# Kernel optimization log

Hardware: AMD Instinct MI355X
Metric: run time of the kernel (lower is better)

## Reference

```python
import jax, jax.numpy as jnp
import numpy as np

T, B, D, H, F, E = 2048, 2, 1024, 16, 4096, 8
HD = D // H


def layer_norm(x, g, b, eps=1e-5):
    m = x.mean(-1, keepdims=True)
    v = ((x - m) ** 2).mean(-1, keepdims=True)
    return (x - m) * jax.lax.rsqrt(v + eps) * g + b


def setup_inputs() -> dict:
    key = jax.random.key(0)
    ks = jax.random.split(key, 24)
    s = 0.02
    inp = {
        "x": jax.random.normal(ks[0], (T, B, D), jnp.float32),
        # self-attention (fairseq MultiheadAttention)
        "Wq": jax.random.normal(ks[1], (D, D), jnp.float32) * s,
        "bq": jnp.zeros((D,), jnp.float32),
        "Wk": jax.random.normal(ks[2], (D, D), jnp.float32) * s,
        "bk": jnp.zeros((D,), jnp.float32),
        "Wv": jax.random.normal(ks[3], (D, D), jnp.float32) * s,
        "bv": jnp.zeros((D,), jnp.float32),
        "Wo": jax.random.normal(ks[4], (D, D), jnp.float32) * s,
        "bo": jnp.zeros((D,), jnp.float32),
        "ln1_g": jnp.ones((D,), jnp.float32),
        "ln1_b": jnp.zeros((D,), jnp.float32),
        "ln2_g": jnp.ones((D,), jnp.float32),
        "ln2_b": jnp.zeros((D,), jnp.float32),
        # MoE: expert_centroids Linear(D -> E, bias=False) => weight [E, D]
        "cent": jax.random.normal(ks[5], (E, D), jnp.float32) * s,
        # per-expert MoESublayer params (base_sublayers=1)
        "e_ln_g": jnp.ones((E, D), jnp.float32),
        "e_ln_b": jnp.zeros((E, D), jnp.float32),
        "e_W1": jax.random.normal(ks[6], (E, D, F), jnp.float32) * s,
        "e_b1": jnp.zeros((E, F), jnp.float32),
        "e_W2": jax.random.normal(ks[7], (E, F, D), jnp.float32) * s,
        "e_b2": jnp.zeros((E, D), jnp.float32),
    }
    return inp


def reference(x, Wq, bq, Wk, bk, Wv, bv, Wo, bo, ln1_g, ln1_b, ln2_g, ln2_b,
              cent, e_ln_g, e_ln_b, e_W1, e_b1, e_W2, e_b2):
    # ---- self-attention block (pre-norm, causal) ----
    res = x  # [T,B,D]
    h = layer_norm(x, ln1_g, ln1_b)
    q = ((h @ Wq) + bq) * (HD ** -0.5)
    k = h @ Wk + bk
    v = h @ Wv + bv
    q = q.reshape(T, B, H, HD)
    k = k.reshape(T, B, H, HD)
    v = v.reshape(T, B, H, HD)
    scores = jnp.einsum('tbhd,sbhd->bhts', q, k)
    causal = jnp.tril(jnp.ones((T, T), bool))
    scores = jnp.where(causal, scores, -1e9)
    p = jax.nn.softmax(scores, axis=-1)
    a = jnp.einsum('bhts,sbhd->tbhd', p, v).reshape(T, B, D)
    x = res + (a @ Wo + bo)

    # ---- MoE block (pre-norm) ----
    res = x
    h = layer_norm(x, ln2_g, ln2_b)
    # MoELayer: transpose(0,1) then flatten -> [B*T, D] token-major by batch
    xs = h.transpose(1, 0, 2).reshape(B * T, D)
    logits = xs.astype(jnp.float32) @ cent.T  # fp32 gating, [N,E]
    assign = jnp.argmax(logits, axis=-1)      # greedy top-1 routing

    # single-device semantics: All2All identity; sort + inverse-sort cancel,
    # so out[t] = expert_{assign[t]}(xs[t]). Compute each expert densely and select.
    def sublayer(g, b, W1, b1, W2, b2):
        hh = jax.nn.relu(layer_norm(xs, g, b) @ W1 + b1)  # [N,F]
        return xs + hh @ W2 + b2                          # internal residual

    ys = jax.vmap(sublayer)(e_ln_g, e_ln_b, e_W1, e_b1, e_W2, e_b2)  # [E,N,D]
    moe_out = jnp.take_along_axis(ys, assign[None, :, None], axis=0)[0]  # [N,D]
    moe_out = moe_out.reshape(B, T, D).transpose(1, 0, 2)  # back to [T,B,D]

    return res + moe_out
```

## Files before the change

### kernel.cpp

```cpp
#include <hip/hip_runtime.h>
#include <hip/hip_bf16.h>
#include <math.h>

#define T_ 2048
#define B_ 2
#define D_ 1024
#define H_ 16
#define F_ 4096
#define E_ 8
#define N_ 4096
#define HD_ 64
#define PADROWS 5120

typedef __attribute__((ext_vector_type(8))) short short8_t;
typedef __attribute__((ext_vector_type(4))) float f32x4_t;
typedef __attribute__((ext_vector_type(16))) float f32x16_t;
typedef __attribute__((ext_vector_type(4))) unsigned u32x4_t;

__device__ __forceinline__ unsigned short f2bf(float f) {
    union { float f; unsigned u; } a; a.f = f;
    unsigned r = a.u + 0x7FFFu + ((a.u >> 16) & 1u);
    return (unsigned short)(r >> 16);
}

__device__ __forceinline__ unsigned cvtpk(float lo, float hi) {
    unsigned r;
    asm("v_cvt_pk_bf16_f32 %0, %1, %2" : "=v"(r) : "v"(lo), "v"(hi));
    return r;
}

__device__ __forceinline__ void glds16(const unsigned short* g, unsigned short* l) {
    __builtin_amdgcn_global_load_lds(
        (const __attribute__((address_space(1))) void*)g,
        (__attribute__((address_space(3))) void*)l, 16, 0, 0);
}

__device__ __forceinline__ void blockReduce2(float& a, float& b, float* sm) {
    #pragma unroll
    for (int m = 32; m; m >>= 1) { a += __shfl_xor(a, m); b += __shfl_xor(b, m); }
    const int w = threadIdx.x >> 6, l = threadIdx.x & 63;
    __syncthreads();
    if (l == 0) { sm[w] = a; sm[8 + w] = b; }
    __syncthreads();
    a = sm[0] + sm[1] + sm[2] + sm[3];
    b = sm[8] + sm[9] + sm[10] + sm[11];
}

__global__ __launch_bounds__(256) void k_transpose4(
    const float* __restrict__ Wq, const float* __restrict__ Wk,
    const float* __restrict__ Wv, const float* __restrict__ Wo,
    unsigned short* __restrict__ WqkvT, unsigned short* __restrict__ WoT) {
    __shared__ float tile[32][33];
    const int zi = blockIdx.z;
    const float* in = zi == 0 ? Wq : (zi == 1 ? Wk : (zi == 2 ? Wv : Wo));
    unsigned short* out = zi == 3 ? WoT : (WqkvT + (size_t)zi * 1024 * 1024);
    const int c0 = blockIdx.x * 32, r0 = blockIdx.y * 32;
    const int tx = threadIdx.x & 31, ty = threadIdx.x >> 5;
    #pragma unroll
    for (int i = 0; i < 32; i += 8)
        tile[ty + i][tx] = in[(size_t)(r0 + ty + i) * 1024 + c0 + tx];
    __syncthreads();
    const int c = threadIdx.x >> 3, rq = (threadIdx.x & 7) * 4;
    ushort4 v;
    v.x = f2bf(tile[rq + 0][c]);
    v.y = f2bf(tile[rq + 1][c]);
    v.z = f2bf(tile[rq + 2][c]);
    v.w = f2bf(tile[rq + 3][c]);
    *(ushort4*)(out + (size_t)(c0 + c) * 1024 + r0 + rq) = v;
}

__global__ __launch_bounds__(256) void k_transpose(const float* __restrict__ in,
                                                   unsigned short* __restrict__ out,
                                                   int R, int C) {
    __shared__ float tile[32][33];
    const int c0 = blockIdx.x * 32, r0 = blockIdx.y * 32;
    const size_t base = (size_t)blockIdx.z * R * C;
    in += base; out += base;
    const int tx = threadIdx.x & 31, ty = threadIdx.x >> 5;
    #pragma unroll
    for (int i = 0; i < 32; i += 8)
        tile[ty + i][tx] = in[(size_t)(r0 + ty + i) * C + c0 + tx];
    __syncthreads();
    const int c = threadIdx.x >> 3, rq = (threadIdx.x & 7) * 4;
    ushort4 v;
    v.x = f2bf(tile[rq + 0][c]);
    v.y = f2bf(tile[rq + 1][c]);
    v.z = f2bf(tile[rq + 2][c]);
    v.w = f2bf(tile[rq + 3][c]);
    *(ushort4*)(out + (size_t)(c0 + c) * R + r0 + rq) = v;
}

__global__ __launch_bounds__(256) void k_transpose_v(const unsigned short* __restrict__ in,
                                                     unsigned short* __restrict__ out) {
    const int bh = blockIdx.x;
    const int t0 = blockIdx.y * 128;
    const int tid = threadIdx.x;
    const int hd = tid & 63;
    const size_t ib = (size_t)bh * T_ * HD_;
    const size_t ob = (size_t)bh * HD_ * T_;
    for (int tb = tid >> 6; tb < 16; tb += 4) {
        const int t = t0 + tb * 8;
        short8_t v;
        #pragma unroll
        for (int k = 0; k < 8; ++k)
            v[k] = (short)in[ib + (size_t)(t + k) * HD_ + hd];
        *(short8_t*)(out + ob + (size_t)hd * T_ + t) = v;
    }
}

__global__ __launch_bounds__(256) void k_ln_x2(const float* __restrict__ x,
                                               const float* __restrict__ g,
                                               const float* __restrict__ b,
                                               const float* __restrict__ bo,
                                               unsigned short* __restrict__ out,
                                               float* __restrict__ x2,
                                               int* __restrict__ counts, int* __restrict__ cursor,
                                               int* __restrict__ perm) {
    __shared__ float sm[16];
    const int row = blockIdx.x, tid = threadIdx.x;
    if (row == 0) {
        if (tid < E_) { counts[tid] = 0; cursor[tid] = 0; }
        for (int i = tid; i < PADROWS; i += 256) perm[i] = -1;
    }
    const float4 v = *(const float4*)(x + (size_t)row * D_ + tid * 4);
    float s1 = v.x + v.y + v.z + v.w;
    float s2 = v.x * v.x + v.y * v.y + v.z * v.z + v.w * v.w;
    blockReduce2(s1, s2, sm);
    const float mean = s1 * (1.f / D_);
    const float inv  = rsqrtf(s2 * (1.f / D_) - mean * mean + 1e-5f);
    const float4 gg = *(const float4*)(g + tid * 4);
    const float4 bb = *(const float4*)(b + tid * 4);
    unsigned long long pk =
          (unsigned long long)f2bf((v.x - mean) * inv * gg.x + bb.x)
        | ((unsigned long long)f2bf((v.y - mean) * inv * gg.y + bb.y) << 16)
        | ((unsigned long long)f2bf((v.z - mean) * inv * gg.z + bb.z) << 32)
        | ((unsigned long long)f2bf((v.w - mean) * inv * gg.w + bb.w) << 48);
    *(unsigned long long*)(out + (size_t)row * D_ + tid * 4) = pk;
    const float4 bv = *(const float4*)(bo + tid * 4);
    float4 o; o.x = v.x + bv.x; o.y = v.y + bv.y; o.z = v.z + bv.z; o.w = v.w + bv.w;
    *(float4*)(x2 + (size_t)row * D_ + tid * 4) = o;
}

__global__ __launch_bounds__(256) void k_init_out(const float* __restrict__ x2u,
                                                  const float* __restrict__ eb2,
                                                  const int* __restrict__ assign,
                                                  float* __restrict__ out) {
    const int row = blockIdx.x, tid = threadIdx.x;
    const int e = assign[row];
    const size_t idx = (size_t)row * D_ + tid * 4;
    const float4 v = *(const float4*)(x2u + idx);
    const float4 b = *(const float4*)(eb2 + (size_t)e * D_ + tid * 4);
    float4 o; o.x = v.x + b.x; o.y = v.y + b.y; o.z = v.z + b.z; o.w = v.w + b.w;
    *(float4*)(out + idx) = o;
}

__device__ __forceinline__ void gemm_core(const unsigned short* ap0, const unsigned short* ap1,
                                          const unsigned short* bp0, const unsigned short* bp1,
                                          int K, unsigned short* Als, unsigned short* Bls,
                                          f32x4_t (&acc)[4][4]) {
    const int tid = threadIdx.x, w = tid >> 6, l = tid & 63;
    const int wm = (w >> 1) * 64, wn = (w & 1) * 64;
    const int fr = l & 15, fg = (l >> 4) * 8;
    const int fgs = fg ^ (((fr >> 1) & 3) << 3);
    f32x4_t z4 = {0.f, 0.f, 0.f, 0.f};
    #pragma unroll
    for (int m = 0; m < 4; m++)
        #pragma unroll
        for (int n = 0; n < 4; n++) acc[m][n] = z4;
    glds16(ap0, Als + w * 512);
    glds16(ap1, Als + (w + 4) * 512);
    glds16(bp0, Bls + w * 512);
    glds16(bp1, Bls + (w + 4) * 512);
    ap0 += 32; ap1 += 32; bp0 += 32; bp1 += 32;
    glds16(ap0, Als + 4096 + w * 512);
    glds16(ap1, Als + 4096 + (w + 4) * 512);
    glds16(bp0, Bls + 4096 + w * 512);
    glds16(bp1, Bls + 4096 + (w + 4) * 512);
    ap0 += 32; ap1 += 32; bp0 += 32; bp1 += 32;
    unsigned c0 = 0, c1 = 4096, c2 = 8192;
    const int nk = K >> 5;
    for (int kt = 0; kt < nk; ++kt) {
        if (kt < nk - 1) asm volatile("s_waitcnt vmcnt(4)" ::: "memory");
        else             asm volatile("s_waitcnt vmcnt(0)" ::: "memory");
        __builtin_amdgcn_s_barrier();
        __builtin_amdgcn_sched_barrier(0);
        if (kt + 2 < nk) {
            glds16(ap0, Als + c2 + w * 512);
            glds16(ap1, Als + c2 + (w + 4) * 512);
            glds16(bp0, Bls + c2 + w * 512);
            glds16(bp1, Bls + c2 + (w + 4) * 512);
            ap0 += 32; ap1 += 32; bp0 += 32; bp1 += 32;
        }
        short8_t a[4], b[4];
        #pragma unroll
        for (int m = 0; m < 4; m++) a[m] = *(const short8_t*)(Als + c0 + (wm + m * 16 + fr) * 32 + fgs);
        #pragma unroll
        for (int n = 0; n < 4; n++) b[n] = *(const short8_t*)(Bls + c0 + (wn + n * 16 + fr) * 32 + fgs);
        __builtin_amdgcn_s_setprio(1);
        #pragma unroll
        for (int m = 0; m < 4; m++)
            #pragma unroll
            for (int n = 0; n < 4; n++)
                acc[m][n] = __builtin_amdgcn_mfma_f32_16x16x32_bf16(a[m], b[n], acc[m][n], 0, 0, 0);
        __builtin_amdgcn_s_setprio(0);
        const unsigned t = c0; c0 = c1; c1 = c2; c2 = t;
    }
}

__global__ __launch_bounds__(256) void k_gemm_qkv(
    const unsigned short* __restrict__ A, const unsigned short* __restrict__ BT,
    const float* __restrict__ bq, const float* __restrict__ bk, const float* __restrict__ bv,
    unsigned short* __restrict__ Qb, unsigned short* __restrict__ Kb, unsigned short* __restrict__ Vb) {
    __shared__ unsigned short Als[12288], Bls[12288];
    const int tid = threadIdx.x, w = tid >> 6, l = tid & 63;
    const int col0 = blockIdx.x * 128, row0 = blockIdx.y * 128;
    const int r0s = w * 16 + (l >> 2), r1s = 64 + w * 16 + (l >> 2);
    const int cs = ((l & 3) ^ ((l >> 3) & 3)) * 8;
    const unsigned short* ap0 = A + (size_t)(row0 + r0s) * D_ + cs;
    const unsigned short* ap1 = A + (size_t)(row0 + r1s) * D_ + cs;
    const unsigned short* bp0 = BT + (size_t)(col0 + r0s) * D_ + cs;
    const unsigned short* bp1 = BT + (size_t)(col0 + r1s) * D_ + cs;
    f32x4_t acc[4][4];
    gemm_core(ap0, ap1, bp0, bp1, D_, Als, Bls, acc);
    const int wm = (w >> 1) * 64, wn = (w & 1) * 64, fr = l & 15, fg4 = l >> 4;
    #pragma unroll
    for (int n = 0; n < 4; n++) {
        const int gcol = col0 + wn + n * 16 + fr;
        const int which = gcol >> 10, dc = gcol & 1023;
        const float bias = which == 0 ? bq[dc] : (which == 1 ? bk[dc] : bv[dc]);
        unsigned short* dst = which == 0 ? Qb : (which == 1 ? Kb : Vb);
        const int hh = dc >> 6, hd = dc & 63;
        #pragma unroll
        for (int m = 0; m < 4; m++)
            #pragma unroll
            for (int rr = 0; rr < 4; rr++) {
                const int grow = row0 + wm + m * 16 + fg4 * 4 + rr;
                float v = acc[m][n][rr] + bias;
                if (which == 0) v *= 0.1803368801111204f;
                const int t = grow >> 1, bb = grow & 1;
                dst[((size_t)(bb * H_ + hh) * T_ + t) * HD_ + hd] = f2bf(v);
            }
    }
}

__global__ __launch_bounds__(256) void k_attn(const unsigned short* __restrict__ Qb,
                                              const unsigned short* __restrict__ Kb,
                                              const unsigned short* __restrict__ Vt,
                                              unsigned short* __restrict__ aout) {
    __shared__ unsigned short Kl[3 * 4096];
    __shared__ unsigned short Vl[3 * 4096];
    const int id = blockIdx.x;
    const int qt = (id < 256) ? (15 - (id & 15)) : (id & 15);
    const int bh = (id >> 4) & 31;
    const int tid = threadIdx.x, w = tid >> 6, l = tid & 63;
    const int q5 = l & 31, hi = l >> 5, l7 = l & 7;
    const int row0 = w * 8 + (l >> 3);
    const int swz = ((l & 7) ^ (l >> 3)) * 8;
    const size_t base = (size_t)bh * T_ * HD_;
    const unsigned short* Qp = Qb + base;
    const unsigned short* kps = Kb + base + (size_t)row0 * HD_ + swz;
    const unsigned short* vps = Vt + base + (size_t)row0 * T_ + swz;
    const int qw0 = qt * 128 + w * 32;
    const int q = qw0 + q5;

    short8_t aq[4];
    #pragma unroll
    for (int khd = 0; khd < 4; ++khd)
        aq[khd] = *(const short8_t*)(Qp + (size_t)q * HD_ + khd * 16 + hi * 8);

    f32x16_t accO0, accO1;
    #pragma unroll
    for (int i = 0; i < 16; ++i) { accO0[i] = 0.f; accO1[i] = 0.f; }
    float mrun = -1e30f, lrun = 0.f;

    const int niter = (qt + 1) * 2;

#define STAGE_KV(t, b) { \
    const size_t ko = (size_t)(t) * 64 * HD_; const int vo = (t) * 64; \
    glds16(kps + ko,            Kl + (b) + w * 512); \
    glds16(kps + ko + 32 * HD_, Kl + (b) + 2048 + w * 512); \
    glds16(vps + vo,            Vl + (b) + w * 512); \
    glds16(vps + vo + 32 * T_,  Vl + (b) + 2048 + w * 512); }

    STAGE_KV(0, 0);
    STAGE_KV(1, 4096);
    unsigned c0 = 0, c1 = 4096, c2 = 8192;

    for (int it = 0; it < niter; ++it) {
        if (it < niter - 1) asm volatile("s_waitcnt vmcnt(4)" ::: "memory");
        else                asm volatile("s_waitcnt vmcnt(0)" ::: "memory");
        __builtin_amdgcn_s_barrier();
        __builtin_amdgcn_sched_barrier(0);
        if (it + 2 < niter) STAGE_KV(it + 2, c2);
        const int s0 = it * 64;
        if (s0 <= qw0 + 31) {
            const unsigned short* KT = Kl + c0;
            const unsigned short* VT = Vl + c0;

            f32x16_t st0, st1;
            #pragma unroll
            for (int i = 0; i < 16; ++i) { st0[i] = 0.f; st1[i] = 0.f; }
            __builtin_amdgcn_s_setprio(1);
            #pragma unroll
            for (int khd = 0; khd < 4; ++khd) {
                const int cb = (khd * 16 + hi * 8) ^ (l7 * 8);
                const short8_t k0 = *(const short8_t*)(KT + q5 * 64 + cb);
                const short8_t k1 = *(const short8_t*)(KT + (32 + q5) * 64 + cb);
                st0 = __builtin_amdgcn_mfma_f32_32x32x16_bf16(k0, aq[khd], st0, 0, 0, 0);
                st1 = __builtin_amdgcn_mfma_f32_32x32x16_bf16(k1, aq[khd], st1, 0, 0, 0);
            }
            __builtin_amdgcn_s_setprio(0);

            const bool domask = (s0 + 63 > qw0);
            float pmax = -3e38f;
            if (domask) {
                #pragma unroll
                for (int r = 0; r < 16; ++r) {
                    const int kv0 = s0 + (r & 3) + 8 * (r >> 2) + 4 * hi;
                    float v0 = st0[r], v1 = st1[r];
                    if (kv0 > q)      v0 = -1e30f;
                    if (kv0 + 32 > q) v1 = -1e30f;
                    st0[r] = v0; st1[r] = v1;
                    pmax = fmaxf(fmaxf(pmax, v0), v1);
                }
            } else {
                #pragma unroll
                for (int r = 0; r < 16; ++r)
                    pmax = fmaxf(fmaxf(pmax, st0[r]), st1[r]);
            }
            pmax = fmaxf(pmax, __shfl_xor(pmax, 32));

            if (!__all(pmax - mrun <= 8.0f)) {
                const float mnew = fmaxf(mrun, pmax);
                const float scl = exp2f(mrun - mnew);
                lrun *= scl;
                #pragma unroll
                for (int i = 0; i < 16; ++i) { accO0[i] *= scl; accO1[i] *= scl; }
                mrun = mnew;
            }

            float pt0[16], pt1[16];
            float rs0 = 0.f, rs1 = 0.f;
            #pragma unroll
            for (int r = 0; r < 16; ++r) {
                pt0[r] = exp2f(st0[r] - mrun);
                pt1[r] = exp2f(st1[r] - mrun);
                rs0 += pt0[r]; rs1 += pt1[r];
            }
            float rs = rs0 + rs1;
            rs += __shfl_xor(rs, 32);
            lrun += rs;

            unsigned Wp[2][4][2];
            #pragma unroll
            for (int b = 0; b < 4; ++b) {
                Wp[0][b][0] = cvtpk(pt0[4 * b + 0], pt0[4 * b + 1]);
                Wp[0][b][1] = cvtpk(pt0[4 * b + 2], pt0[4 * b + 3]);
                Wp[1][b][0] = cvtpk(pt1[4 * b + 0], pt1[4 * b + 1]);
                Wp[1][b][1] = cvtpk(pt1[4 * b + 2], pt1[4 * b + 3]);
            }

            __builtin_amdgcn_s_setprio(1);
            #pragma unroll
            for (int ks = 0; ks < 4; ++ks) {
                const int t = ks >> 1, b0 = (ks & 1) * 2;
                const unsigned ownA0 = Wp[t][b0][0],     ownA1 = Wp[t][b0][1];
                const unsigned ownB0 = Wp[t][b0 + 1][0], ownB1 = Wp[t][b0 + 1][1];
                const unsigned send0 = hi ? ownA0 : ownB0;
                const unsigned send1 = hi ? ownA1 : ownB1;
                const unsigned recv0 = __shfl_xor(send0, 32);
                const unsigned recv1 = __shfl_xor(send1, 32);
                u32x4_t wds;
                wds[0] = hi ? recv0 : ownA0;
                wds[1] = hi ? recv1 : ownA1;
                wds[2] = hi ? ownB0 : recv0;
                wds[3] = hi ? ownB1 : recv1;
                const short8_t pfrag = __builtin_bit_cast(short8_t, wds);
                const int cb = (ks * 16 + hi * 8) ^ (l7 * 8);
                const short8_t v0 = *(const short8_t*)(VT + q5 * 64 + cb);
                const short8_t v1 = *(const short8_t*)(VT + (32 + q5) * 64 + cb);
                accO0 = __builtin_amdgcn_mfma_f32_32x32x16_bf16(v0, pfrag, accO0, 0, 0, 0);
                accO1 = __builtin_amdgcn_mfma_f32_32x32x16_bf16(v1, pfrag, accO1, 0, 0, 0);
            }
            __builtin_amdgcn_s_setprio(0);
        }
        const unsigned tb = c0; c0 = c1; c1 = c2; c2 = tb;
    }
#undef STAGE_KV

    const float linv = 1.f / lrun;
    const int bidx = bh >> 4, hidx = bh & 15;
    unsigned short* orow = aout + (size_t)(q * B_ + bidx) * D_ + hidx * 64;
    #pragma unroll
    for (int g = 0; g < 4; ++g) {
        const int hd0 = 8 * g + 4 * hi;
        unsigned long long pk0 =
              (unsigned long long)f2bf(accO0[4 * g + 0] * linv)
            | ((unsigned long long)f2bf(accO0[4 * g + 1] * linv) << 16)
            | ((unsigned long long)f2bf(accO0[4 * g + 2] * linv) << 32)
            | ((unsigned long long)f2bf(accO0[4 * g + 3] * linv) << 48);
        *(unsigned long long*)(orow + hd0) = pk0;
        unsigned long long pk1 =
              (unsigned long long)f2bf(accO1[4 * g + 0] * linv)
            | ((unsigned long long)f2bf(accO1[4 * g + 1] * linv) << 16)
            | ((unsigned long long)f2bf(accO1[4 * g + 2] * linv) << 32)
            | ((unsigned long long)f2bf(accO1[4 * g + 3] * linv) << 48);
        *(unsigned long long*)(orow + 32 + hd0) = pk1;
    }
}

__global__ __launch_bounds__(256) void k_gemm_o(
    const unsigned short* __restrict__ A, const unsigned short* __restrict__ BT,
    float* __restrict__ x2) {
    __shared__ unsigned short Als[12288], Bls[12288];
    const int tid = threadIdx.x, w = tid >> 6, l = tid & 63;
    const int row0 = blockIdx.x * 128, col0 = blockIdx.y * 128;
    const int kc = blockIdx.z * 512;
    const int r0s = w * 16 + (l >> 2), r1s = 64 + w * 16 + (l >> 2);
    const int cs = ((l & 3) ^ ((l >> 3) & 3)) * 8;
    const unsigned short* ap0 = A + (size_t)(row0 + r0s) * D_ + kc + cs;
    const unsigned short* ap1 = A + (size_t)(row0 + r1s) * D_ + kc + cs;
    const unsigned short* bp0 = BT + (size_t)(col0 + r0s) * D_ + kc + cs;
    const unsigned short* bp1 = BT + (size_t)(col0 + r1s) * D_ + kc + cs;
    f32x4_t acc[4][4];
    gemm_core(ap0, ap1, bp0, bp1, 512, Als, Bls, acc);
    const int wm = (w >> 1) * 64, wn = (w & 1) * 64, fr = l & 15, fg4 = l >> 4;
    #pragma unroll
    for (int n = 0; n < 4; n++) {
        const int gcol = col0 + wn + n * 16 + fr;
        #pragma unroll
        for (int m = 0; m < 4; m++)
            #pragma unroll
            for (int rr = 0; rr < 4; rr++) {
                const int grow = row0 + wm + m * 16 + fg4 * 4 + rr;
                atomicAdd(&x2[(size_t)grow * D_ + gcol], acc[m][n][rr]);
            }
    }
}

__global__ __launch_bounds__(256) void k_ln2_gate(
    float* __restrict__ x2, const float* __restrict__ g2, const float* __restrict__ b2,
    const float* __restrict__ cent, const float* __restrict__ eg, const float* __restrict__ eb,
    unsigned short* __restrict__ z, int* __restrict__ assign, int* __restrict__ counts) {
    __shared__ float sm[48];
    const int row = blockIdx.x, tid = threadIdx.x;
    const int w = tid >> 6, l = tid & 63;
    float* xr = x2 + (size_t)row * D_;
    const float4 v = *(const float4*)(xr + tid * 4);
    float s1 = v.x + v.y + v.z + v.w;
    float s2 = v.x * v.x + v.y * v.y + v.z * v.z + v.w * v.w;
    blockReduce2(s1, s2, sm);
    const float mean = s1 * (1.f / D_);
    const float inv  = rsqrtf(s2 * (1.f / D_) - mean * mean + 1e-5f);
    const float4 gg = *(const float4*)(g2 + tid * 4), bb = *(const float4*)(b2 + tid * 4);
    float4 u;
    u.x = (v.x - mean) * inv * gg.x + bb.x;
    u.y = (v.y - mean) * inv * gg.y + bb.y;
    u.z = (v.z - mean) * inv * gg.z + bb.z;
    u.w = (v.w - mean) * inv * gg.w + bb.w;
    float p[E_];
    #pragma unroll
    for (int e = 0; e < E_; e++) {
        const float4 c = *(const float4*)(cent + (size_t)e * D_ + tid * 4);
        p[e] = u.x * c.x + u.y * c.y + u.z * c.z + u.w * c.w;
    }
    #pragma unroll
    for (int m = 32; m; m >>= 1)
        #pragma unroll
        for (int e = 0; e < E_; e++) p[e] += __shfl_xor(p[e], m);
    __syncthreads();
    if (l == 0) {
        #pragma unroll
        for (int e = 0; e < E_; e++) sm[16 + e * 4 + w] = p[e];
    }
    __syncthreads();
    int best = 0; float bl = -1e30f;
    #pragma unroll
    for (int e = 0; e < E_; e++) {
        const float le = sm[16 + e * 4] + sm[16 + e * 4 + 1] + sm[16 + e * 4 + 2] + sm[16 + e * 4 + 3];
        if (le > bl) { bl = le; best = e; }
    }
    float t1 = u.x + u.y + u.z + u.w;
    float t2 = u.x * u.x + u.y * u.y + u.z * u.z + u.w * u.w;
    blockReduce2(t1, t2, sm);
    const float m2   = t1 * (1.f / D_);
    const float inv2 = rsqrtf(t2 * (1.f / D_) - m2 * m2 + 1e-5f);
    const float4 egv = *(const float4*)(eg + (size_t)best * D_ + tid * 4);
    const float4 ebv = *(const float4*)(eb + (size_t)best * D_ + tid * 4);
    unsigned long long pk =
          (unsigned long long)f2bf((u.x - m2) * inv2 * egv.x + ebv.x)
        | ((unsigned long long)f2bf((u.y - m2) * inv2 * egv.y + ebv.y) << 16)
        | ((unsigned long long)f2bf((u.z - m2) * inv2 * egv.z + ebv.z) << 32)
        | ((unsigned long long)f2bf((u.w - m2) * inv2 * egv.w + ebv.w) << 48);
    *(unsigned long long*)(z + (size_t)row * D_ + tid * 4) = pk;
    float4 xu; xu.x = v.x + u.x; xu.y = v.y + u.y; xu.z = v.z + u.z; xu.w = v.w + u.w;
    *(float4*)(xr + tid * 4) = xu;
    if (tid == 0) { assign[row] = best; atomicAdd(&counts[best], 1); }
}

__global__ void k_offsets(const int* counts, int* pad_off) {
    if (threadIdx.x == 0) {
        int o = 0; pad_off[0] = 0;
        for (int e = 0; e < E_; e++) { o += ((counts[e] + 127) >> 7) << 7; pad_off[e + 1] = o; }
    }
}

__global__ void k_scatter(const int* assign, const int* pad_off, int* cursor, int* perm) {
    const int r = blockIdx.x * 256 + threadIdx.x;
    if (r >= N_) return;
    const int e = assign[r];
    const int pos = pad_off[e] + atomicAdd(&cursor[e], 1);
    perm[pos] = r;
}

__global__ __launch_bounds__(256) void k_gemm_e1(
    const unsigned short* __restrict__ z, const unsigned short* __restrict__ W1T,
    const float* __restrict__ eb1, const int* __restrict__ pad_off,
    const int* __restrict__ perm, unsigned short* __restrict__ Y1) {
    __shared__ unsigned short Als[12288], Bls[12288];
    const int tid = threadIdx.x, w = tid >> 6, l = tid & 63;
    const int col0 = blockIdx.x * 128, row0 = blockIdx.y * 128;
    if (row0 >= pad_off[E_]) return;
    int e = 0;
    while (row0 >= pad_off[e + 1]) e++;
    const int r0s = w * 16 + (l >> 2), r1s = 64 + w * 16 + (l >> 2);
    const int cs = ((l & 3) ^ ((l >> 3) & 3)) * 8;
    int pr0 = perm[row0 + r0s]; if (pr0 < 0) pr0 = 0;
    int pr1 = perm[row0 + r1s]; if (pr1 < 0) pr1 = 0;
    const unsigned short* ap0 = z + (size_t)pr0 * D_ + cs;
    const unsigned short* ap1 = z + (size_t)pr1 * D_ + cs;
    const unsigned short* BTe = W1T + (size_t)e * F_ * D_;
    const unsigned short* bp0 = BTe + (size_t)(col0 + r0s) * D_ + cs;
    const unsigned short* bp1 = BTe + (size_t)(col0 + r1s) * D_ + cs;
    f32x4_t acc[4][4];
    gemm_core(ap0, ap1, bp0, bp1, D_, Als, Bls, acc);
    const float* b1e = eb1 + (size_t)e * F_;
    const int wm = (w >> 1) * 64, wn = (w & 1) * 64, fr = l & 15, fg4 = l >> 4;
    #pragma unroll
    for (int n = 0; n < 4; n++) {
        const int gcol = col0 + wn + n * 16 + fr;
        const float bias = b1e[gcol];
        #pragma unroll
        for (int m = 0; m < 4; m++)
            #pragma unroll
            for (int rr = 0; rr < 4; rr++) {
                const int grow = row0 + wm + m * 16 + fg4 * 4 + rr;
                Y1[(size_t)grow * F_ + gcol] = f2bf(fmaxf(acc[m][n][rr] + bias, 0.f));
            }
    }
}

__global__ __launch_bounds__(256) void k_gemm_e2(
    const unsigned short* __restrict__ Y1, const unsigned short* __restrict__ W2T,
    const int* __restrict__ pad_off, const int* __restrict__ perm,
    float* __restrict__ out) {
    __shared__ unsigned short Als[12288], Bls[12288];
    const int tid = threadIdx.x, w = tid >> 6, l = tid & 63;
    const int row0 = blockIdx.x * 128, col0 = blockIdx.y * 128;
    const int kc = blockIdx.z * 2048;
    if (row0 >= pad_off[E_]) return;
    int e = 0;
    while (row0 >= pad_off[e + 1]) e++;
    const int r0s = w * 16 + (l >> 2), r1s = 64 + w * 16 + (l >> 2);
    const int cs = ((l & 3) ^ ((l >> 3) & 3)) * 8;
    const unsigned short* ap0 = Y1 + (size_t)(row0 + r0s) * F_ + kc + cs;
    const unsigned short* ap1 = Y1 + (size_t)(row0 + r1s) * F_ + kc + cs;
    const unsigned short* BTe = W2T + (size_t)e * D_ * F_;
    const unsigned short* bp0 = BTe + (size_t)(col0 + r0s) * F_ + kc + cs;
    const unsigned short* bp1 = BTe + (size_t)(col0 + r1s) * F_ + kc + cs;
    f32x4_t acc[4][4];
    gemm_core(ap0, ap1, bp0, bp1, 2048, Als, Bls, acc);
    const int wm = (w >> 1) * 64, wn = (w & 1) * 64, fr = l & 15, fg4 = l >> 4;
    #pragma unroll
    for (int n = 0; n < 4; n++) {
        const int gcol = col0 + wn + n * 16 + fr;
        #pragma unroll
        for (int m = 0; m < 4; m++)
            #pragma unroll
            for (int rr = 0; rr < 4; rr++) {
                const int grow = row0 + wm + m * 16 + fg4 * 4 + rr;
                const int rdst = perm[grow];
                if (rdst >= 0)
                    atomicAdd(&out[(size_t)rdst * D_ + gcol], acc[m][n][rr]);
            }
    }
}

extern "C" void kernel_launch(void* const* d_in, const int* in_sizes, int n_in,
                              void* d_out, int out_size, void* d_ws, size_t ws_size,
                              hipStream_t stream) {
    const float* x    = (const float*)d_in[0];
    const float* Wq   = (const float*)d_in[1];
    const float* bq   = (const float*)d_in[2];
    const float* Wk   = (const float*)d_in[3];
    const float* bk   = (const float*)d_in[4];
    const float* Wv   = (const float*)d_in[5];
    const float* bv   = (const float*)d_in[6];
    const float* Wo   = (const float*)d_in[7];
    const float* bo   = (const float*)d_in[8];
    const float* ln1g = (const float*)d_in[9];
    const float* ln1b = (const float*)d_in[10];
    const float* ln2g = (const float*)d_in[11];
    const float* ln2b = (const float*)d_in[12];
    const float* cent = (const float*)d_in[13];
    const float* egw  = (const float*)d_in[14];
    const float* ebw  = (const float*)d_in[15];
    const float* eW1  = (const float*)d_in[16];
    const float* eb1  = (const float*)d_in[17];
    const float* eW2  = (const float*)d_in[18];
    const float* eb2  = (const float*)d_in[19];
    float* out = (float*)d_out;

    char* W = (char*)d_ws;
    unsigned short* WqkvT = (unsigned short*)(W);
    unsigned short* WoT   = (unsigned short*)(W + 6291456);
    unsigned short* Qb    = (unsigned short*)(W + 8388608);
    unsigned short* Kb    = (unsigned short*)(W + 16777216);
    unsigned short* Vb    = (unsigned short*)(W + 25165824);
    unsigned short* aout  = (unsigned short*)(W + 33554432);
    unsigned short* Y1    = (unsigned short*)(W);
    unsigned short* W1T   = (unsigned short*)(W + 41943040);
    unsigned short* W2T   = (unsigned short*)(W + 109051904);
    unsigned short* h1z   = (unsigned short*)(W + 176160768);
    float*          x2    = (float*)(W + 184549376);
    unsigned short* Vt    = (unsigned short*)(W + 201326592);
    int*            assign= (int*)(W + 209715200);
    int*            perm  = (int*)(W + 209731584);
    int*            counts= (int*)(W + 209752064);
    int*            cursor= (int*)(W + 209752192);
    int*            pad_off=(int*)(W + 209752320);

    k_transpose4<<<dim3(32, 32, 4), 256, 0, stream>>>(Wq, Wk, Wv, Wo, WqkvT, WoT);
    k_transpose<<<dim3(128, 32, 8), 256, 0, stream>>>(eW1, W1T, 1024, 4096);
    k_transpose<<<dim3(32, 128, 8), 256, 0, stream>>>(eW2, W2T, 4096, 1024);

    k_ln_x2<<<N_, 256, 0, stream>>>(x, ln1g, ln1b, bo, h1z, x2, counts, cursor, perm);
    k_gemm_qkv<<<dim3(24, 32), 256, 0, stream>>>(h1z, WqkvT, bq, bk, bv, Qb, Kb, Vb);
    k_transpose_v<<<dim3(32, 16), 256, 0, stream>>>(Vb, Vt);
    k_attn<<<dim3(512), 256, 0, stream>>>(Qb, Kb, Vt, aout);
    k_gemm_o<<<dim3(32, 8, 2), 256, 0, stream>>>(aout, WoT, x2);
    k_ln2_gate<<<N_, 256, 0, stream>>>(x2, ln2g, ln2b, cent, egw, ebw, h1z, assign, counts);
    k_offsets<<<1, 64, 0, stream>>>(counts, pad_off);
    k_scatter<<<16, 256, 0, stream>>>(assign, pad_off, cursor, perm);
    k_init_out<<<N_, 256, 0, stream>>>(x2, eb2, assign, out);
    k_gemm_e1<<<dim3(32, 40), 256, 0, stream>>>(h1z, W1T, eb1, pad_off, perm, Y1);
    k_gemm_e2<<<dim3(40, 8, 2), 256, 0, stream>>>(Y1, W2T, pad_off, perm, out);
}
```

Before: 464.2 us.

## Load A operand directly to registers in expert down-projection GEMM, triple-buffer B in LDS

The second expert GEMM no longer stages the Y1 activation tile through shared memory. Each wave now reads its A fragments straight from global memory into registers, double-buffered across k-steps, while only the W2T tile goes through LDS with a three-stage rotating buffer and explicit vmcnt waits. This cuts LDS traffic and halves LDS footprint, which may raise occupancy. In exchange it relies on uncoalesced-ish direct global fragment loads and hand-tuned wait counts that must match the issued loads.

```diff
diff --git a/kernel.cpp b/kernel.cpp
--- a/kernel.cpp
+++ b/kernel.cpp
@@ -554,7 +554,7 @@
     const unsigned short* __restrict__ Y1, const unsigned short* __restrict__ W2T,
     const int* __restrict__ pad_off, const int* __restrict__ perm,
     float* __restrict__ out) {
-    __shared__ unsigned short Als[12288], Bls[12288];
+    __shared__ unsigned short Bls[3 * 4096];
     const int tid = threadIdx.x, w = tid >> 6, l = tid & 63;
     const int row0 = blockIdx.x * 128, col0 = blockIdx.y * 128;
     const int kc = blockIdx.z * 2048;
@@ -563,14 +563,89 @@
     while (row0 >= pad_off[e + 1]) e++;
     const int r0s = w * 16 + (l >> 2), r1s = 64 + w * 16 + (l >> 2);
     const int cs = ((l & 3) ^ ((l >> 3) & 3)) * 8;
-    const unsigned short* ap0 = Y1 + (size_t)(row0 + r0s) * F_ + kc + cs;
-    const unsigned short* ap1 = Y1 + (size_t)(row0 + r1s) * F_ + kc + cs;
+    const int wm = (w >> 1) * 64, wn = (w & 1) * 64;
+    const int fr = l & 15, fg = (l >> 4) * 8;
+    const int fgs = fg ^ (((fr >> 1) & 3) << 3);
     const unsigned short* BTe = W2T + (size_t)e * D_ * F_;
     const unsigned short* bp0 = BTe + (size_t)(col0 + r0s) * F_ + kc + cs;
     const unsigned short* bp1 = BTe + (size_t)(col0 + r1s) * F_ + kc + cs;
+    const unsigned short* aP0 = Y1 + (size_t)(row0 + wm +  0 + fr) * F_ + kc + fg;
+    const unsigned short* aP1 = Y1 + (size_t)(row0 + wm + 16 + fr) * F_ + kc + fg;
+    const unsigned short* aP2 = Y1 + (size_t)(row0 + wm + 32 + fr) * F_ + kc + fg;
+    const unsigned short* aP3 = Y1 + (size_t)(row0 + wm + 48 + fr) * F_ + kc + fg;
+    f32x4_t z4 = {0.f, 0.f, 0.f, 0.f};
     f32x4_t acc[4][4];
-    gemm_core(ap0, ap1, bp0, bp1, 2048, Als, Bls, acc);
-    const int wm = (w >> 1) * 64, wn = (w & 1) * 64, fr = l & 15, fg4 = l >> 4;
+    #pragma unroll
+    for (int m = 0; m < 4; m++)
+        #pragma unroll
+        for (int n = 0; n < 4; n++) acc[m][n] = z4;
+    glds16(bp0, Bls + w * 512); glds16(bp1, Bls + (w + 4) * 512); bp0 += 32; bp1 += 32;
+    short8_t aA0 = *(const short8_t*)aP0; aP0 += 32;
+    short8_t aA1 = *(const short8_t*)aP1; aP1 += 32;
+    short8_t aA2 = *(const short8_t*)aP2; aP2 += 32;
+    short8_t aA3 = *(const short8_t*)aP3; aP3 += 32;
+    glds16(bp0, Bls + 4096 + w * 512); glds16(bp1, Bls + 4096 + (w + 4) * 512); bp0 += 32; bp1 += 32;
+    short8_t aB0, aB1, aB2, aB3;
+    unsigned c0 = 0, c1 = 4096, c2 = 8192;
+    const int nk = 64;
+    for (int kt = 0; kt < nk; kt += 2) {
+        asm volatile("s_waitcnt vmcnt(2)" ::: "memory");
+        __builtin_amdgcn_s_barrier();
+        __builtin_amdgcn_sched_barrier(0);
+        aB0 = *(const short8_t*)aP0; aP0 += 32;
+        aB1 = *(const short8_t*)aP1; aP1 += 32;
+        aB2 = *(const short8_t*)aP2; aP2 += 32;
+        aB3 = *(const short8_t*)aP3; aP3 += 32;
+        if (kt + 2 < nk) {
+            glds16(bp0, Bls + c2 + w * 512); glds16(bp1, Bls + c2 + (w + 4) * 512);
+            bp0 += 32; bp1 += 32;
+        }
+        {
+            short8_t b[4];
+            #pragma unroll
+            for (int n = 0; n < 4; n++) b[n] = *(const short8_t*)(Bls + c0 + (wn + n * 16 + fr) * 32 + fgs);
+            __builtin_amdgcn_s_setprio(1);
+            #pragma unroll
+            for (int n = 0; n < 4; n++) {
+                acc[0][n] = __builtin_amdgcn_mfma_f32_16x16x32_bf16(aA0, b[n], acc[0][n], 0, 0, 0);
+                acc[1][n] = __builtin_amdgcn_mfma_f32_16x16x32_bf16(aA1, b[n], acc[1][n], 0, 0, 0);
+                acc[2][n] = __builtin_amdgcn_mfma_f32_16x16x32_bf16(aA2, b[n], acc[2][n], 0, 0, 0);
+                acc[3][n] = __builtin_amdgcn_mfma_f32_16x16x32_bf16(aA3, b[n], acc[3][n], 0, 0, 0);
+            }
+            __builtin_amdgcn_s_setprio(0);
+        }
+        { const unsigned t = c0; c0 = c1; c1 = c2; c2 = t; }
+        if (kt + 1 < nk - 1) asm volatile("s_waitcnt vmcnt(2)" ::: "memory");
+        else                 asm volatile("s_waitcnt vmcnt(0)" ::: "memory");
+        __builtin_amdgcn_s_barrier();
+        __builtin_amdgcn_sched_barrier(0);
+        if (kt + 2 < nk) {
+            aA0 = *(const short8_t*)aP0; aP0 += 32;
+            aA1 = *(const short8_t*)aP1; aP1 += 32;
+            aA2 = *(const short8_t*)aP2; aP2 += 32;
+            aA3 = *(const short8_t*)aP3; aP3 += 32;
+        }
+        if (kt + 3 < nk) {
+            glds16(bp0, Bls + c2 + w * 512); glds16(bp1, Bls + c2 + (w + 4) * 512);
+            bp0 += 32; bp1 += 32;
+        }
+        {
+            short8_t b[4];
+            #pragma unroll
+            for (int n = 0; n < 4; n++) b[n] = *(const short8_t*)(Bls + c0 + (wn + n * 16 + fr) * 32 + fgs);
+            __builtin_amdgcn_s_setprio(1);
+            #pragma unroll
+            for (int n = 0; n < 4; n++) {
+                acc[0][n] = __builtin_amdgcn_mfma_f32_16x16x32_bf16(aB0, b[n], acc[0][n], 0, 0, 0);
+                acc[1][n] = __builtin_amdgcn_mfma_f32_16x16x32_bf16(aB1, b[n], acc[1][n], 0, 0, 0);
+                acc[2][n] = __builtin_amdgcn_mfma_f32_16x16x32_bf16(aB2, b[n], acc[2][n], 0, 0, 0);
+                acc[3][n] = __builtin_amdgcn_mfma_f32_16x16x32_bf16(aB3, b[n], acc[3][n], 0, 0, 0);
+            }
+            __builtin_amdgcn_s_setprio(0);
+        }
+        { const unsigned t = c0; c0 = c1; c1 = c2; c2 = t; }
+    }
+    const int fg4 = l >> 4;
     #pragma unroll
     for (int n = 0; n < 4; n++) {
         const int gcol = col0 + wn + n * 16 + fr;
```

Result: slower. 544.0 us (+17.2%).
